# Kernel optimization log

Measured on AMD Instinct MI355X. Metric: run time of the kernel, lower is better.

## Reference

```python
import jax, jax.numpy as jnp
import numpy as np

BS, IN, H, G, E, A = 4096, 256, 256, 64, 256, 30
NW = IN * H  # hypernet-generated weight count per sample


def _ln(x, g, b, eps=1e-5):
    mu = jnp.mean(x, axis=-1, keepdims=True)
    var = jnp.mean(jnp.square(x - mu), axis=-1, keepdims=True)
    return (x - mu) * jax.lax.rsqrt(var + eps) * g + b


def setup_inputs() -> dict:
    key = jax.random.key(0)
    ks = jax.random.split(key, 24)
    sc = 0.02
    return {
        "inputs": jax.random.normal(ks[0], (BS, IN), jnp.float32),
        "hidden_state": jax.random.normal(ks[1], (BS, H), jnp.float32),
        "goal": jax.random.normal(ks[2], (BS, G), jnp.float32),
        "ln1_g": jnp.ones((IN,), jnp.float32),
        "ln1_b": jnp.zeros((IN,), jnp.float32),
        "hy_w1": jax.random.normal(ks[3], (E, G), jnp.float32) * sc,
        "hy_b1": jnp.zeros((E,), jnp.float32),
        "hy_w2": jax.random.normal(ks[4], (NW + H, E), jnp.float32) * sc,
        "hy_b2": jnp.zeros((NW + H,), jnp.float32),
        "ln2_g": jnp.ones((H,), jnp.float32),
        "ln2_b": jnp.zeros((H,), jnp.float32),
        "fe_w": jax.random.normal(ks[5], (H, H), jnp.float32) * sc,
        "fe_b": jnp.zeros((H,), jnp.float32),
        "w_ih": jax.random.normal(ks[6], (3 * H, H), jnp.float32) * sc,
        "w_hh": jax.random.normal(ks[7], (3 * H, H), jnp.float32) * sc,
        "b_ih": jnp.zeros((3 * H,), jnp.float32),
        "b_hh": jnp.zeros((3 * H,), jnp.float32),
        "val_w": jax.random.normal(ks[8], (1, H), jnp.float32) * sc,
        "val_b": jnp.zeros((1,), jnp.float32),
        "adv_w": jax.random.normal(ks[9], (A, H), jnp.float32) * sc,
        "adv_b": jnp.zeros((A,), jnp.float32),
    }


def reference(inputs, hidden_state, goal, ln1_g, ln1_b, hy_w1, hy_b1, hy_w2, hy_b2,
              ln2_g, ln2_b, fe_w, fe_b, w_ih, w_hh, b_ih, b_hh, val_w, val_b,
              adv_w, adv_b):
    x_in = _ln(inputs, ln1_g, ln1_b)  # [BS, IN]
    # hypernetwork: goal -> per-sample (weights, bias)
    h1 = jax.nn.relu(goal @ hy_w1.T + hy_b1)           # [BS, E]
    hyper = jnp.tanh(h1 @ hy_w2.T + hy_b2) * 3.0        # [BS, NW+H]
    weights = hyper[:, :NW].reshape(BS, IN, H)
    bias = hyper[:, NW:]                                 # [BS, H]
    x = jnp.einsum('bi,bih->bh', x_in, weights) + bias   # per-sample matmul
    x = _ln(x, ln2_g, ln2_b)
    x = jax.nn.relu(x) @ fe_w.T + fe_b                    # feat_extract_2
    # GRUCell
    h_in = hidden_state.reshape(-1, H)
    gi = x @ w_ih.T + b_ih
    gh = h_in @ w_hh.T + b_hh
    i_r, i_z, i_n = jnp.split(gi, 3, axis=1)
    h_r, h_z, h_n = jnp.split(gh, 3, axis=1)
    r = jax.nn.sigmoid(i_r + h_r)
    z = jax.nn.sigmoid(i_z + h_z)
    n = jnp.tanh(i_n + r * h_n)
    h = (1.0 - z) * n + z * h_in
    # dueling heads
    val = h @ val_w.T + val_b                             # [BS, 1]
    adv = h @ adv_w.T + adv_b                             # [BS, A]
    q = val + (adv - jnp.mean(adv, axis=1, keepdims=True))
    return q, h
```

## Files before the change

### kernel.cpp

```cpp
#include <hip/hip_runtime.h>
#include <hip/hip_bf16.h>

typedef unsigned short u16;
typedef __attribute__((ext_vector_type(4))) float f32x4;
typedef __attribute__((ext_vector_type(8))) short short8;
typedef __attribute__((ext_vector_type(8))) u16 u16x8;

__device__ __forceinline__ f32x4 fzero() { f32x4 z = {0.f, 0.f, 0.f, 0.f}; return z; }

__device__ __forceinline__ u16 f2b(float x) {
  unsigned u = __builtin_bit_cast(unsigned, x);
  unsigned r = (u + 0x7fffu + ((u >> 16) & 1u)) >> 16;
  return (u16)r;
}

#define BS 4096
#define H_ 256
#define A_ 30

#define OFF_W2B   0UL
#define OFF_HIDB  33685504UL
#define OFF_FWT   35782656UL
#define OFF_WIHB  35913728UL
#define OFF_WHHB  36306944UL
#define OFF_H1B   36700160UL
#define OFF_XIN   38797312UL
#define OFF_WCB   40894464UL
#define OFF_BCB   41287680UL
#define OFF_PART  42991616UL

#define NC_W2   2105344L
#define NC_HID  131072L
#define NC_FET  8192L
#define NC_WIH  24576L
#define NC_WHH  24576L
#define NB_CONV 8960
#define NB_PRE  (NB_CONV + 4096 + 4096)

__device__ __forceinline__ void blk_ln(float v, float* red, int t, float& mu, float& inv) {
  float s = v, sq = v * v;
  #pragma unroll
  for (int o = 32; o; o >>= 1) { s += __shfl_xor(s, o); sq += __shfl_xor(sq, o); }
  int w = t >> 6;
  if ((t & 63) == 0) { red[w] = s; red[4 + w] = sq; }
  __syncthreads();
  float S = red[0] + red[1] + red[2] + red[3];
  float Q = red[4] + red[5] + red[6] + red[7];
  mu = S * (1.f / 256.f);
  float var = Q * (1.f / 256.f) - mu * mu;
  inv = rsqrtf(var + 1e-5f);
  __syncthreads();
}

__global__ void k_pre(const float* __restrict__ hyw2, const float* __restrict__ hid,
                      const float* __restrict__ few,  const float* __restrict__ wih,
                      const float* __restrict__ whh,
                      const float* __restrict__ inp,  const float* __restrict__ ln1g,
                      const float* __restrict__ ln1b,
                      const float* __restrict__ goal, const float* __restrict__ hyw1,
                      const float* __restrict__ hyb1,
                      u16* __restrict__ w2b, u16* __restrict__ hidb, u16* __restrict__ fwbT,
                      u16* __restrict__ wihb, u16* __restrict__ whhb,
                      float* __restrict__ xin, u16* __restrict__ h1b) {
  const int bx = blockIdx.x, t = threadIdx.x;
  __shared__ float sm[64];

  if (bx < NB_CONV) {
    long c = (long)bx * 256 + t;
    if (c < NC_W2) {
      long d = c * 8;
      int kk0 = (int)((c & 3) * 8);
      int h   = (int)((c >> 2) & 255);
      long s  = c >> 10;
      int ks  = (int)(s & 7);
      long i  = s >> 3;
      const float* src = hyw2 + (i * 256 + h) * 256 + ks * 32 + kk0;
      f32x4 a = *(const f32x4*)src;
      f32x4 b = *(const f32x4*)(src + 4);
      u16x8 o;
      o[0]=f2b(a[0]); o[1]=f2b(a[1]); o[2]=f2b(a[2]); o[3]=f2b(a[3]);
      o[4]=f2b(b[0]); o[5]=f2b(b[1]); o[6]=f2b(b[2]); o[7]=f2b(b[3]);
      *(u16x8*)(w2b + d) = o;
      return;
    }
    c -= NC_W2;
    const float* src = nullptr; u16* dst = nullptr;
    if (c < NC_HID) { src = hid; dst = hidb; }
    else {
      c -= NC_HID;
      if (c < NC_FET) {
        long d = c * 8;
        int h = (int)(c >> 5), e0 = (int)((c & 31) * 8);
        u16x8 o;
        #pragma unroll
        for (int j = 0; j < 8; ++j) o[j] = f2b(few[(long)(e0 + j) * 256 + h]);
        *(u16x8*)(fwbT + d) = o;
        return;
      }
      c -= NC_FET;
      if (c < NC_WIH) { src = wih; dst = wihb; }
      else { c -= NC_WIH; src = whh; dst = whhb; }
    }
    long e = c * 8;
    f32x4 a = *(const f32x4*)(src + e);
    f32x4 b = *(const f32x4*)(src + e + 4);
    u16x8 o;
    o[0]=f2b(a[0]); o[1]=f2b(a[1]); o[2]=f2b(a[2]); o[3]=f2b(a[3]);
    o[4]=f2b(b[0]); o[5]=f2b(b[1]); o[6]=f2b(b[2]); o[7]=f2b(b[3]);
    *(u16x8*)(dst + e) = o;
    return;
  }

  if (bx < NB_CONV + 4096) {
    int bb = bx - NB_CONV;
    float v = inp[(long)bb * 256 + t];
    float mu, inv; blk_ln(v, sm, t, mu, inv);
    xin[(long)bb * 256 + t] = (v - mu) * inv * ln1g[t] + ln1b[t];
    return;
  }

  {
    int bb = bx - (NB_CONV + 4096);
    if (t < 64) sm[t] = goal[(long)bb * 64 + t];
    __syncthreads();
    const float* wr = hyw1 + (long)t * 64;
    float acc = hyb1[t];
    #pragma unroll
    for (int g4 = 0; g4 < 16; ++g4) {
      f32x4 w = *(const f32x4*)(wr + g4 * 4);
      acc = fmaf(sm[g4*4+0], w[0], acc);
      acc = fmaf(sm[g4*4+1], w[1], acc);
      acc = fmaf(sm[g4*4+2], w[2], acc);
      acc = fmaf(sm[g4*4+3], w[3], acc);
    }
    h1b[(long)bb * 256 + t] = f2b(fmaxf(acc, 0.f));
  }
}

__global__ __launch_bounds__(256, 2) void k_big(const u16* __restrict__ w2b,
                                                const u16* __restrict__ h1b,
                                                const float* __restrict__ xin,
                                                const float* __restrict__ b2,
                                                float* __restrict__ part) {
  const int bx = blockIdx.x;
  const int islice = bx & 7, btile = bx >> 3;
  const int b0 = btile * 64, i0 = islice * 32;
  const int ni = (islice == 7) ? 33 : 32;
  const int t = threadIdx.x, lane = t & 63, wid = t >> 6;
  const int la = lane & 15, lb = lane >> 4;
  const int c0 = wid * 64;

  __shared__ u16 As[64 * 264];
  __shared__ float xs[32][64];

  #pragma unroll
  for (int j = 0; j < 8; ++j) {
    int q = t + 256 * j;
    int row = q >> 5, cc = q & 31;
    *(u16x8*)&As[row * 264 + cc * 8] = *(const u16x8*)(h1b + (long)(b0 + row) * 256 + cc * 8);
  }
  {
    int row = t >> 2, part4 = t & 3;
    const float* src = xin + (long)(b0 + row) * 256 + i0 + part4 * 8;
    f32x4 v0 = *(const f32x4*)src;
    f32x4 v1 = *(const f32x4*)(src + 4);
    #pragma unroll
    for (int j = 0; j < 4; ++j) xs[part4 * 8 + j][row] = v0[j];
    #pragma unroll
    for (int j = 0; j < 4; ++j) xs[part4 * 8 + 4 + j][row] = v1[j];
  }
  __syncthreads();

  const u16* bptr = w2b + (long)i0 * 8 * 8192 + (c0 + la) * 32 + lb * 8;
  const int lds_a = la * 528 + lb * 16;

  f32x4 accT[4][4];
  #pragma unroll
  for (int m = 0; m < 4; ++m)
    #pragma unroll
    for (int n = 0; n < 4; ++n) accT[m][n] = fzero();

  short8 bf[4][4];
  #pragma unroll
  for (int s = 0; s < 4; ++s)
    #pragma unroll
    for (int n = 0; n < 4; ++n)
      bf[s][n] = *(const short8*)(bptr + (long)s * 8192 + n * 512);

  for (int ii = 0; ii < ni; ++ii) {
    f32x4 cf[4][4];
    #pragma unroll
    for (int ks = 0; ks < 8; ++ks) {
      const int s = ii * 8 + ks;
      __builtin_amdgcn_s_barrier();
      short8 af[4];
      #pragma unroll
      for (int m = 0; m < 4; ++m)
        af[m] = *(const short8*)((const char*)As + lds_a + m * 8448 + ks * 64);
      __builtin_amdgcn_s_setprio(1);
      if (ks == 0) {
        #pragma unroll
        for (int m = 0; m < 4; ++m)
          #pragma unroll
          for (int n = 0; n < 4; ++n)
            cf[m][n] = __builtin_amdgcn_mfma_f32_16x16x32_bf16(af[m], bf[ks & 3][n], fzero(), 0, 0, 0);
      } else {
        #pragma unroll
        for (int m = 0; m < 4; ++m)
          #pragma unroll
          for (int n = 0; n < 4; ++n)
            cf[m][n] = __builtin_amdgcn_mfma_f32_16x16x32_bf16(af[m], bf[ks & 3][n], cf[m][n], 0, 0, 0);
      }
      __builtin_amdgcn_s_setprio(0);
      #pragma unroll
      for (int n = 0; n < 4; ++n)
        bf[ks & 3][n] = *(const short8*)(bptr + (long)(s + 4) * 8192 + n * 512);
    }
    const int ig = i0 + ii;
    const bool isb = (ig == 256);
    f32x4 xv[4];
    if (isb) {
      #pragma unroll
      for (int m = 0; m < 4; ++m) { f32x4 o = {1.f,1.f,1.f,1.f}; xv[m] = o; }
    } else {
      #pragma unroll
      for (int m = 0; m < 4; ++m)
        xv[m] = *(const f32x4*)&xs[ii][m * 16 + lb * 4];
    }
    float b2v[4];
    #pragma unroll
    for (int n = 0; n < 4; ++n)
      b2v[n] = b2[(long)ig * 256 + c0 + n * 16 + la];
    #pragma unroll
    for (int m = 0; m < 4; ++m)
      #pragma unroll
      for (int n = 0; n < 4; ++n)
        #pragma unroll
        for (int r = 0; r < 4; ++r) {
          float pre = cf[m][n][r] + b2v[n];
          float t2 = pre * pre;
          float w = pre * fmaf(t2, fmaf(t2, fmaf(t2, -0.161905f, 0.4f), -1.0f), 3.0f);
          accT[m][n][r] = fmaf(xv[m][r], w, accT[m][n][r]);
        }
  }

  float* dst = part + (long)islice * (4096 * 256);
  #pragma unroll
  for (int m = 0; m < 4; ++m)
    #pragma unroll
    for (int n = 0; n < 4; ++n)
      #pragma unroll
      for (int r = 0; r < 4; ++r)
        __builtin_nontemporal_store(accT[m][n][r],
            &dst[(long)(b0 + m * 16 + lb * 4 + r) * 256 + (c0 + n * 16 + la)]);
}

__global__ void k_mid(const float* __restrict__ part, const float* __restrict__ g,
                      const float* __restrict__ b, u16* __restrict__ yb,
                      const float* __restrict__ wihf, const float* __restrict__ few,
                      u16* __restrict__ wcb,
                      const float* __restrict__ bih, const float* __restrict__ feb,
                      float* __restrict__ bcb) {
  const int bx = blockIdx.x, t = threadIdx.x;
  __shared__ float sm[256];
  if (bx < 4096) {
    float s = 0.f;
    #pragma unroll
    for (int sl = 0; sl < 8; ++sl) s += part[(long)sl * (4096 * 256) + (long)bx * 256 + t];
    float mu, inv; blk_ln(s, sm, t, mu, inv);
    float v = (s - mu) * inv * g[t] + b[t];
    yb[(long)bx * 256 + t] = f2b(fmaxf(v, 0.f));
    return;
  }
  if (bx < 4096 + 768) {
    int gg = bx - 4096;
    sm[t] = wihf[(long)gg * 256 + t];
    __syncthreads();
    float acc = 0.f;
    #pragma unroll 8
    for (int e = 0; e < 256; ++e) acc = fmaf(sm[e], few[(long)e * 256 + t], acc);
    wcb[(long)gg * 256 + t] = f2b(acc);
    return;
  }
  {
    int gg = (bx - 4864) * 256 + t;
    float acc = bih[gg];
    const float* wr = wihf + (long)gg * 256;
    #pragma unroll 8
    for (int e = 0; e < 256; ++e) acc = fmaf(wr[e], feb[e], acc);
    bcb[gg] = acc;
  }
}

__device__ __forceinline__ void gemm256(const u16* __restrict__ Ab, const u16* __restrict__ Bb,
                                        const float* __restrict__ bias, float* __restrict__ Cf,
                                        int N, int ntiles, int blk, u16* As, u16* Bs) {
  const int t = threadIdx.x;
  const int mt = blk / ntiles, nt = blk % ntiles;
  const int m0 = mt * 128, n0 = nt * 128;
  const int lane = t & 63, wid = t >> 6;
  const int la = lane & 15, lb = lane >> 4;
  const int r0 = (wid >> 1) * 64, c0 = (wid & 1) * 64;
  f32x4 acc[4][4];
  #pragma unroll
  for (int m = 0; m < 4; ++m)
    #pragma unroll
    for (int n = 0; n < 4; ++n) acc[m][n] = fzero();
  for (int kh = 0; kh < 2; ++kh) {
    #pragma unroll
    for (int j = 0; j < 8; ++j) {
      int q = t + 256 * j;
      int row = q >> 4, cc = q & 15;
      *(u16x8*)&As[row * 136 + cc * 8] = *(const u16x8*)(Ab + (long)(m0 + row) * 256 + kh * 128 + cc * 8);
      *(u16x8*)&Bs[row * 136 + cc * 8] = *(const u16x8*)(Bb + (long)(n0 + row) * 256 + kh * 128 + cc * 8);
    }
    __syncthreads();
    #pragma unroll
    for (int ks = 0; ks < 4; ++ks) {
      short8 af[4], bf[4];
      #pragma unroll
      for (int m = 0; m < 4; ++m) af[m] = *(const short8*)&As[(r0 + m * 16 + la) * 136 + ks * 32 + lb * 8];
      #pragma unroll
      for (int n = 0; n < 4; ++n) bf[n] = *(const short8*)&Bs[(c0 + n * 16 + la) * 136 + ks * 32 + lb * 8];
      #pragma unroll
      for (int m = 0; m < 4; ++m)
        #pragma unroll
        for (int n = 0; n < 4; ++n)
          acc[m][n] = __builtin_amdgcn_mfma_f32_16x16x32_bf16(af[m], bf[n], acc[m][n], 0, 0, 0);
    }
    __syncthreads();
  }
  #pragma unroll
  for (int n = 0; n < 4; ++n) {
    int gc = n0 + c0 + n * 16 + la;
    float bv = bias[gc];
    #pragma unroll
    for (int m = 0; m < 4; ++m) {
      int gr = m0 + r0 + m * 16 + lb * 4;
      #pragma unroll
      for (int r = 0; r < 4; ++r)
        Cf[(long)(gr + r) * N + gc] = acc[m][n][r] + bv;
    }
  }
}

__global__ __launch_bounds__(256) void k_gigh(const u16* __restrict__ yb, const u16* __restrict__ wcb,
                                              const float* __restrict__ bcb,
                                              const u16* __restrict__ hidb, const u16* __restrict__ whhb,
                                              const float* __restrict__ bhh,
                                              float* __restrict__ gim, float* __restrict__ ghm) {
  __shared__ u16 smem[2 * 128 * 136];
  const int bx = blockIdx.x;
  if (bx < 192) gemm256(yb,   wcb,  bcb, gim, 768, 6, bx,       smem, smem + 128 * 136);
  else          gemm256(hidb, whhb, bhh, ghm, 768, 6, bx - 192, smem, smem + 128 * 136);
}

__global__ void k_gru(const float* __restrict__ gi, const float* __restrict__ gh,
                      const float* __restrict__ hin,
                      const float* __restrict__ vw, const float* __restrict__ vb,
                      const float* __restrict__ aw, const float* __restrict__ ab,
                      float* __restrict__ qout, float* __restrict__ hout) {
  int bb = blockIdx.x, t = threadIdx.x;
  const float* gib = gi + (long)bb * 768;
  const float* ghb = gh + (long)bb * 768;
  float ir = gib[t], iz = gib[256 + t], inx = gib[512 + t];
  float hr = ghb[t], hz = ghb[256 + t], hn = ghb[512 + t];
  float hprev = hin[(long)bb * 256 + t];
  float r = 1.f / (1.f + expf(-(ir + hr)));
  float z = 1.f / (1.f + expf(-(iz + hz)));
  float n = tanhf(inx + r * hn);
  float h = (1.f - z) * n + z * hprev;
  hout[(long)bb * 256 + t] = h;
  __shared__ float hl[256];
  __shared__ float ov[32];
  __shared__ float mred;
  hl[t] = h;
  __syncthreads();
  int gidx = t >> 3, lg = t & 7;
  if (gidx < 31) {
    const float* wr = (gidx < 30) ? (aw + (long)gidx * 256) : vw;
    float p = 0.f;
    #pragma unroll 8
    for (int j = 0; j < 32; ++j) p += hl[lg + 8 * j] * wr[lg + 8 * j];
    p += __shfl_xor(p, 1); p += __shfl_xor(p, 2); p += __shfl_xor(p, 4);
    if (lg == 0) ov[gidx] = p + ((gidx < 30) ? ab[gidx] : vb[0]);
  }
  __syncthreads();
  if (t == 0) {
    float m = 0.f;
    #pragma unroll
    for (int a = 0; a < 30; ++a) m += ov[a];
    mred = m * (1.f / 30.f);
  }
  __syncthreads();
  if (t < 30) qout[(long)bb * 30 + t] = ov[30] + ov[t] - mred;
}

extern "C" void kernel_launch(void* const* d_in, const int* in_sizes, int n_in,
                              void* d_out, int out_size, void* d_ws, size_t ws_size,
                              hipStream_t stream) {
  const float* inputs = (const float*)d_in[0];
  const float* hidden = (const float*)d_in[1];
  const float* goal   = (const float*)d_in[2];
  const float* ln1g   = (const float*)d_in[3];
  const float* ln1b   = (const float*)d_in[4];
  const float* hyw1   = (const float*)d_in[5];
  const float* hyb1   = (const float*)d_in[6];
  const float* hyw2   = (const float*)d_in[7];
  const float* hyb2   = (const float*)d_in[8];
  const float* ln2g   = (const float*)d_in[9];
  const float* ln2b   = (const float*)d_in[10];
  const float* few    = (const float*)d_in[11];
  const float* feb    = (const float*)d_in[12];
  const float* wih    = (const float*)d_in[13];
  const float* whh    = (const float*)d_in[14];
  const float* bih    = (const float*)d_in[15];
  const float* bhh    = (const float*)d_in[16];
  const float* valw   = (const float*)d_in[17];
  const float* valb   = (const float*)d_in[18];
  const float* advw   = (const float*)d_in[19];
  const float* advb   = (const float*)d_in[20];

  char* ws = (char*)d_ws;
  u16* w2b   = (u16*)(ws + OFF_W2B);
  u16* hidb  = (u16*)(ws + OFF_HIDB);
  u16* fwbT  = (u16*)(ws + OFF_FWT);
  u16* wihb  = (u16*)(ws + OFF_WIHB);
  u16* whhb  = (u16*)(ws + OFF_WHHB);
  u16* h1b   = (u16*)(ws + OFF_H1B);
  float* xin = (float*)(ws + OFF_XIN);
  u16* yb    = (u16*)(ws + OFF_XIN);
  u16* wcb   = (u16*)(ws + OFF_WCB);
  float* bcb = (float*)(ws + OFF_BCB);
  float* prt = (float*)(ws + OFF_PART);
  float* gim = (float*)(ws + OFF_PART);
  float* ghm = (float*)(ws + OFF_PART + 12582912UL);
  float* qout = (float*)d_out;
  float* hout = qout + (long)BS * A_;

  k_pre<<<NB_PRE, 256, 0, stream>>>(hyw2, hidden, few, wih, whh,
                                    inputs, ln1g, ln1b, goal, hyw1, hyb1,
                                    w2b, hidb, fwbT, wihb, whhb, xin, h1b);
  k_big<<<512, 256, 0, stream>>>(w2b, h1b, xin, hyb2, prt);
  k_mid<<<4867, 256, 0, stream>>>(prt, ln2g, ln2b, yb, wih, few, wcb, bih, feb, bcb);
  k_gigh<<<384, 256, 0, stream>>>(yb, wcb, bcb, hidb, whhb, bhh, gim, ghm);
  k_gru<<<4096, 256, 0, stream>>>(gim, ghm, hidden, valw, valb, advw, advb, qout, hout);
}
```

Measured before the change: 376.1 us.

## Fuse LN2, GRU gate GEMMs, GRU cell and dueling heads into one kernel

Replaces the separate k_mid, k_gigh and k_gru kernels with a single k_post kernel. Each 16-row tile sums the partials, applies LN2+ReLU, runs both gate GEMMs with MFMA against pre-fragmented bf16 weights, applies the GRU cell and computes the dueling heads, so the gi/gh intermediates never go to global memory. The folded W_ih·fe_w weight and bias are now built inside k_pre, and the bf16 copy of the hidden state is made in shared memory instead. k_big also moves the x/bias loads and barrier to the top of each i-iteration. The risk is that k_post launches only 256 blocks, which may underuse the GPU, and its B-fragments are read directly from global memory.

```diff
diff --git a/kernel.cpp b/kernel.cpp
--- a/kernel.cpp
+++ b/kernel.cpp
@@ -15,27 +15,23 @@
 }
 
 #define BS 4096
-#define H_ 256
 #define A_ 30
 
 #define OFF_W2B   0UL
-#define OFF_HIDB  33685504UL
-#define OFF_FWT   35782656UL
-#define OFF_WIHB  35913728UL
-#define OFF_WHHB  36306944UL
-#define OFF_H1B   36700160UL
-#define OFF_XIN   38797312UL
-#define OFF_WCB   40894464UL
-#define OFF_BCB   41287680UL
-#define OFF_PART  42991616UL
+#define OFF_H1B   33685504UL
+#define OFF_XIN   35782656UL
+#define OFF_WCFR  39976960UL
+#define OFF_WHFR  40370176UL
+#define OFF_BC    40763392UL
+#define OFF_PART  40766464UL
 
 #define NC_W2   2105344L
-#define NC_HID  131072L
-#define NC_FET  8192L
-#define NC_WIH  24576L
-#define NC_WHH  24576L
-#define NB_CONV 8960
-#define NB_PRE  (NB_CONV + 4096 + 4096)
+#define NB_W2   8224
+#define NB_WHH  96
+#define NB_LN1  4096
+#define NB_H1   4096
+#define NB_WC   768
+#define NB_PRE  (NB_W2 + NB_WHH + NB_LN1 + NB_H1 + NB_WC)
 
 __device__ __forceinline__ void blk_ln(float v, float* red, int t, float& mu, float& inv) {
   float s = v, sq = v * v;
@@ -52,75 +48,59 @@
   __syncthreads();
 }
 
-__global__ void k_pre(const float* __restrict__ hyw2, const float* __restrict__ hid,
-                      const float* __restrict__ few,  const float* __restrict__ wih,
-                      const float* __restrict__ whh,
+__global__ void k_pre(const float* __restrict__ hyw2, const float* __restrict__ whh,
                       const float* __restrict__ inp,  const float* __restrict__ ln1g,
                       const float* __restrict__ ln1b,
                       const float* __restrict__ goal, const float* __restrict__ hyw1,
                       const float* __restrict__ hyb1,
-                      u16* __restrict__ w2b, u16* __restrict__ hidb, u16* __restrict__ fwbT,
-                      u16* __restrict__ wihb, u16* __restrict__ whhb,
-                      float* __restrict__ xin, u16* __restrict__ h1b) {
+                      const float* __restrict__ wih,  const float* __restrict__ few,
+                      const float* __restrict__ feb,  const float* __restrict__ bih,
+                      u16* __restrict__ w2b, u16* __restrict__ whfr,
+                      float* __restrict__ xin, u16* __restrict__ h1b,
+                      u16* __restrict__ wcfr, float* __restrict__ bcv) {
   const int bx = blockIdx.x, t = threadIdx.x;
-  __shared__ float sm[64];
-
-  if (bx < NB_CONV) {
+  __shared__ float sm[256];
+  __shared__ float red[8];
+
+  if (bx < NB_W2) {
     long c = (long)bx * 256 + t;
-    if (c < NC_W2) {
-      long d = c * 8;
-      int kk0 = (int)((c & 3) * 8);
-      int h   = (int)((c >> 2) & 255);
-      long s  = c >> 10;
-      int ks  = (int)(s & 7);
-      long i  = s >> 3;
-      const float* src = hyw2 + (i * 256 + h) * 256 + ks * 32 + kk0;
-      f32x4 a = *(const f32x4*)src;
-      f32x4 b = *(const f32x4*)(src + 4);
-      u16x8 o;
-      o[0]=f2b(a[0]); o[1]=f2b(a[1]); o[2]=f2b(a[2]); o[3]=f2b(a[3]);
-      o[4]=f2b(b[0]); o[5]=f2b(b[1]); o[6]=f2b(b[2]); o[7]=f2b(b[3]);
-      *(u16x8*)(w2b + d) = o;
-      return;
-    }
-    c -= NC_W2;
-    const float* src = nullptr; u16* dst = nullptr;
-    if (c < NC_HID) { src = hid; dst = hidb; }
-    else {
-      c -= NC_HID;
-      if (c < NC_FET) {
-        long d = c * 8;
-        int h = (int)(c >> 5), e0 = (int)((c & 31) * 8);
-        u16x8 o;
-        #pragma unroll
-        for (int j = 0; j < 8; ++j) o[j] = f2b(few[(long)(e0 + j) * 256 + h]);
-        *(u16x8*)(fwbT + d) = o;
-        return;
-      }
-      c -= NC_FET;
-      if (c < NC_WIH) { src = wih; dst = wihb; }
-      else { c -= NC_WIH; src = whh; dst = whhb; }
-    }
-    long e = c * 8;
-    f32x4 a = *(const f32x4*)(src + e);
-    f32x4 b = *(const f32x4*)(src + e + 4);
+    long d = c * 8;
+    int kk0 = (int)((c & 3) * 8);
+    int h   = (int)((c >> 2) & 255);
+    long s  = c >> 10;
+    int ks  = (int)(s & 7);
+    long i  = s >> 3;
+    const float* src = hyw2 + (i * 256 + h) * 256 + ks * 32 + kk0;
+    f32x4 a = *(const f32x4*)src;
+    f32x4 b = *(const f32x4*)(src + 4);
     u16x8 o;
     o[0]=f2b(a[0]); o[1]=f2b(a[1]); o[2]=f2b(a[2]); o[3]=f2b(a[3]);
     o[4]=f2b(b[0]); o[5]=f2b(b[1]); o[6]=f2b(b[2]); o[7]=f2b(b[3]);
-    *(u16x8*)(dst + e) = o;
+    *(u16x8*)(w2b + d) = o;
     return;
   }
-
-  if (bx < NB_CONV + 4096) {
-    int bb = bx - NB_CONV;
+  if (bx < NB_W2 + NB_WHH) {
+    int c = (bx - NB_W2) * 256 + t;
+    int ks = c / 3072, rem = c - ks * 3072;
+    int g = rem >> 2, kk0 = (rem & 3) * 8;
+    const float* src = whh + (long)g * 256 + ks * 32 + kk0;
+    f32x4 a = *(const f32x4*)src;
+    f32x4 b = *(const f32x4*)(src + 4);
+    u16x8 o;
+    o[0]=f2b(a[0]); o[1]=f2b(a[1]); o[2]=f2b(a[2]); o[3]=f2b(a[3]);
+    o[4]=f2b(b[0]); o[5]=f2b(b[1]); o[6]=f2b(b[2]); o[7]=f2b(b[3]);
+    *(u16x8*)(whfr + ((long)ks * 768 + g) * 32 + kk0) = o;
+    return;
+  }
+  if (bx < NB_W2 + NB_WHH + NB_LN1) {
+    int bb = bx - (NB_W2 + NB_WHH);
     float v = inp[(long)bb * 256 + t];
-    float mu, inv; blk_ln(v, sm, t, mu, inv);
+    float mu, inv; blk_ln(v, red, t, mu, inv);
     xin[(long)bb * 256 + t] = (v - mu) * inv * ln1g[t] + ln1b[t];
     return;
   }
-
-  {
-    int bb = bx - (NB_CONV + 4096);
+  if (bx < NB_W2 + NB_WHH + NB_LN1 + NB_H1) {
+    int bb = bx - (NB_W2 + NB_WHH + NB_LN1);
     if (t < 64) sm[t] = goal[(long)bb * 64 + t];
     __syncthreads();
     const float* wr = hyw1 + (long)t * 64;
@@ -134,6 +114,22 @@
       acc = fmaf(sm[g4*4+3], w[3], acc);
     }
     h1b[(long)bb * 256 + t] = f2b(fmaxf(acc, 0.f));
+    return;
+  }
+  {
+    int gg = bx - (NB_W2 + NB_WHH + NB_LN1 + NB_H1);
+    sm[t] = wih[(long)gg * 256 + t];
+    __syncthreads();
+    float acc = 0.f;
+    #pragma unroll 8
+    for (int e = 0; e < 256; ++e) acc = fmaf(sm[e], few[(long)e * 256 + t], acc);
+    wcfr[((long)(t >> 5) * 768 + gg) * 32 + (t & 31)] = f2b(acc);
+    float p = sm[t] * feb[t];
+    #pragma unroll
+    for (int o = 32; o; o >>= 1) p += __shfl_xor(p, o);
+    if ((t & 63) == 0) red[t >> 6] = p;
+    __syncthreads();
+    if (t == 0) bcv[gg] = bih[gg] + red[0] + red[1] + red[2] + red[3];
   }
 }
 
@@ -188,11 +184,27 @@
       bf[s][n] = *(const short8*)(bptr + (long)s * 8192 + n * 512);
 
   for (int ii = 0; ii < ni; ++ii) {
+    __builtin_amdgcn_s_barrier();
+    const int ig = i0 + ii;
+    const bool isb = (ig == 256);
+    f32x4 xv[4];
+    if (isb) {
+      #pragma unroll
+      for (int m = 0; m < 4; ++m) { f32x4 o = {1.f,1.f,1.f,1.f}; xv[m] = o; }
+    } else {
+      #pragma unroll
+      for (int m = 0; m < 4; ++m)
+        xv[m] = *(const f32x4*)&xs[ii][m * 16 + lb * 4];
+    }
+    float b2v[4];
+    #pragma unroll
+    for (int n = 0; n < 4; ++n)
+      b2v[n] = b2[(long)ig * 256 + c0 + n * 16 + la];
+
     f32x4 cf[4][4];
     #pragma unroll
     for (int ks = 0; ks < 8; ++ks) {
       const int s = ii * 8 + ks;
-      __builtin_amdgcn_s_barrier();
       short8 af[4];
       #pragma unroll
       for (int m = 0; m < 4; ++m)
@@ -216,21 +228,6 @@
       for (int n = 0; n < 4; ++n)
         bf[ks & 3][n] = *(const short8*)(bptr + (long)(s + 4) * 8192 + n * 512);
     }
-    const int ig = i0 + ii;
-    const bool isb = (ig == 256);
-    f32x4 xv[4];
-    if (isb) {
-      #pragma unroll
-      for (int m = 0; m < 4; ++m) { f32x4 o = {1.f,1.f,1.f,1.f}; xv[m] = o; }
-    } else {
-      #pragma unroll
-      for (int m = 0; m < 4; ++m)
-        xv[m] = *(const f32x4*)&xs[ii][m * 16 + lb * 4];
-    }
-    float b2v[4];
-    #pragma unroll
-    for (int n = 0; n < 4; ++n)
-      b2v[n] = b2[(long)ig * 256 + c0 + n * 16 + la];
     #pragma unroll
     for (int m = 0; m < 4; ++m)
       #pragma unroll
@@ -255,145 +252,160 @@
             &dst[(long)(b0 + m * 16 + lb * 4 + r) * 256 + (c0 + n * 16 + la)]);
 }
 
-__global__ void k_mid(const float* __restrict__ part, const float* __restrict__ g,
-                      const float* __restrict__ b, u16* __restrict__ yb,
-                      const float* __restrict__ wihf, const float* __restrict__ few,
-                      u16* __restrict__ wcb,
-                      const float* __restrict__ bih, const float* __restrict__ feb,
-                      float* __restrict__ bcb) {
+__global__ __launch_bounds__(256) void k_post(const float* __restrict__ part,
+                                              const float* __restrict__ ln2g,
+                                              const float* __restrict__ ln2b,
+                                              const u16* __restrict__ wcfr,
+                                              const u16* __restrict__ whfr,
+                                              const float* __restrict__ bcv,
+                                              const float* __restrict__ bhh,
+                                              const float* __restrict__ hidden,
+                                              const float* __restrict__ advw,
+                                              const float* __restrict__ advb,
+                                              const float* __restrict__ valw,
+                                              const float* __restrict__ valb,
+                                              float* __restrict__ qout,
+                                              float* __restrict__ hout) {
   const int bx = blockIdx.x, t = threadIdx.x;
-  __shared__ float sm[256];
-  if (bx < 4096) {
-    float s = 0.f;
-    #pragma unroll
-    for (int sl = 0; sl < 8; ++sl) s += part[(long)sl * (4096 * 256) + (long)bx * 256 + t];
-    float mu, inv; blk_ln(s, sm, t, mu, inv);
-    float v = (s - mu) * inv * g[t] + b[t];
-    yb[(long)bx * 256 + t] = f2b(fmaxf(v, 0.f));
-    return;
-  }
-  if (bx < 4096 + 768) {
-    int gg = bx - 4096;
-    sm[t] = wihf[(long)gg * 256 + t];
-    __syncthreads();
-    float acc = 0.f;
-    #pragma unroll 8
-    for (int e = 0; e < 256; ++e) acc = fmaf(sm[e], few[(long)e * 256 + t], acc);
-    wcb[(long)gg * 256 + t] = f2b(acc);
-    return;
-  }
-  {
-    int gg = (bx - 4864) * 256 + t;
-    float acc = bih[gg];
-    const float* wr = wihf + (long)gg * 256;
-    #pragma unroll 8
-    for (int e = 0; e < 256; ++e) acc = fmaf(wr[e], feb[e], acc);
-    bcb[gg] = acc;
-  }
-}
-
-__device__ __forceinline__ void gemm256(const u16* __restrict__ Ab, const u16* __restrict__ Bb,
-                                        const float* __restrict__ bias, float* __restrict__ Cf,
-                                        int N, int ntiles, int blk, u16* As, u16* Bs) {
-  const int t = threadIdx.x;
-  const int mt = blk / ntiles, nt = blk % ntiles;
-  const int m0 = mt * 128, n0 = nt * 128;
+  const int b0 = bx * 16;
+  __shared__ u16 ya[16 * 264];
+  __shared__ u16 ha[16 * 264];
+  __shared__ float hs[16 * 264];
+  __shared__ float ov[16][33];
+  __shared__ float ms[16];
+
+  {
+    const int r = t >> 4, ch = (t & 15) * 16;
+    const float* pb = part + (long)(b0 + r) * 256 + ch;
+    f32x4 s4[4];
+    #pragma unroll
+    for (int q = 0; q < 4; ++q) s4[q] = fzero();
+    #pragma unroll
+    for (int sl = 0; sl < 8; ++sl) {
+      const f32x4* ps = (const f32x4*)(pb + (long)sl * (4096 * 256));
+      #pragma unroll
+      for (int q = 0; q < 4; ++q) {
+        f32x4 v = __builtin_nontemporal_load(ps + q);
+        s4[q] += v;
+      }
+    }
+    float sv = 0.f, sq = 0.f;
+    #pragma unroll
+    for (int q = 0; q < 4; ++q)
+      #pragma unroll
+      for (int j = 0; j < 4; ++j) { float v = s4[q][j]; sv += v; sq += v * v; }
+    #pragma unroll
+    for (int o = 1; o < 16; o <<= 1) { sv += __shfl_xor(sv, o); sq += __shfl_xor(sq, o); }
+    float mu = sv * (1.f / 256.f);
+    float inv = rsqrtf(sq * (1.f / 256.f) - mu * mu + 1e-5f);
+    u16x8 o0, o1;
+    #pragma unroll
+    for (int q = 0; q < 4; ++q)
+      #pragma unroll
+      for (int j = 0; j < 4; ++j) {
+        int c = ch + q * 4 + j;
+        float v = (s4[q][j] - mu) * inv * ln2g[c] + ln2b[c];
+        v = fmaxf(v, 0.f);
+        if (q < 2) o0[q * 4 + j] = f2b(v); else o1[(q - 2) * 4 + j] = f2b(v);
+      }
+    *(u16x8*)&ya[r * 264 + ch] = o0;
+    *(u16x8*)&ya[r * 264 + ch + 8] = o1;
+  }
+  {
+    const int r = t >> 4, ch = (t & 15) * 16;
+    const float* hp = hidden + (long)(b0 + r) * 256 + ch;
+    u16x8 o0, o1;
+    #pragma unroll
+    for (int j = 0; j < 8; ++j) o0[j] = f2b(hp[j]);
+    #pragma unroll
+    for (int j = 0; j < 8; ++j) o1[j] = f2b(hp[8 + j]);
+    *(u16x8*)&ha[r * 264 + ch] = o0;
+    *(u16x8*)&ha[r * 264 + ch + 8] = o1;
+  }
+  __syncthreads();
+
   const int lane = t & 63, wid = t >> 6;
   const int la = lane & 15, lb = lane >> 4;
-  const int r0 = (wid >> 1) * 64, c0 = (wid & 1) * 64;
-  f32x4 acc[4][4];
-  #pragma unroll
-  for (int m = 0; m < 4; ++m)
-    #pragma unroll
-    for (int n = 0; n < 4; ++n) acc[m][n] = fzero();
-  for (int kh = 0; kh < 2; ++kh) {
-    #pragma unroll
-    for (int j = 0; j < 8; ++j) {
-      int q = t + 256 * j;
-      int row = q >> 4, cc = q & 15;
-      *(u16x8*)&As[row * 136 + cc * 8] = *(const u16x8*)(Ab + (long)(m0 + row) * 256 + kh * 128 + cc * 8);
-      *(u16x8*)&Bs[row * 136 + cc * 8] = *(const u16x8*)(Bb + (long)(n0 + row) * 256 + kh * 128 + cc * 8);
-    }
-    __syncthreads();
-    #pragma unroll
-    for (int ks = 0; ks < 4; ++ks) {
-      short8 af[4], bf[4];
-      #pragma unroll
-      for (int m = 0; m < 4; ++m) af[m] = *(const short8*)&As[(r0 + m * 16 + la) * 136 + ks * 32 + lb * 8];
-      #pragma unroll
-      for (int n = 0; n < 4; ++n) bf[n] = *(const short8*)&Bs[(c0 + n * 16 + la) * 136 + ks * 32 + lb * 8];
-      #pragma unroll
-      for (int m = 0; m < 4; ++m)
-        #pragma unroll
-        for (int n = 0; n < 4; ++n)
-          acc[m][n] = __builtin_amdgcn_mfma_f32_16x16x32_bf16(af[m], bf[n], acc[m][n], 0, 0, 0);
-    }
-    __syncthreads();
-  }
+  const int c0w = wid * 64;
+  f32x4 aR[4], aZ[4], aN[4], aH[4];
+  #pragma unroll
+  for (int n = 0; n < 4; ++n) { aR[n] = fzero(); aZ[n] = fzero(); aN[n] = fzero(); aH[n] = fzero(); }
+  #pragma unroll
+  for (int ks = 0; ks < 8; ++ks) {
+    short8 ay = *(const short8*)&ya[la * 264 + ks * 32 + lb * 8];
+    short8 ah = *(const short8*)&ha[la * 264 + ks * 32 + lb * 8];
+    #pragma unroll
+    for (int n = 0; n < 4; ++n) {
+      const int c = c0w + n * 16 + la;
+      const u16* wp = wcfr + ((long)ks * 768 + c) * 32 + lb * 8;
+      const u16* hp = whfr + ((long)ks * 768 + c) * 32 + lb * 8;
+      short8 bWr = *(const short8*)wp;
+      short8 bWz = *(const short8*)(wp + 256 * 32);
+      short8 bWn = *(const short8*)(wp + 512 * 32);
+      short8 bHr = *(const short8*)hp;
+      short8 bHz = *(const short8*)(hp + 256 * 32);
+      short8 bHn = *(const short8*)(hp + 512 * 32);
+      aR[n] = __builtin_amdgcn_mfma_f32_16x16x32_bf16(ay, bWr, aR[n], 0, 0, 0);
+      aR[n] = __builtin_amdgcn_mfma_f32_16x16x32_bf16(ah, bHr, aR[n], 0, 0, 0);
+      aZ[n] = __builtin_amdgcn_mfma_f32_16x16x32_bf16(ay, bWz, aZ[n], 0, 0, 0);
+      aZ[n] = __builtin_amdgcn_mfma_f32_16x16x32_bf16(ah, bHz, aZ[n], 0, 0, 0);
+      aN[n] = __builtin_amdgcn_mfma_f32_16x16x32_bf16(ay, bWn, aN[n], 0, 0, 0);
+      aH[n] = __builtin_amdgcn_mfma_f32_16x16x32_bf16(ah, bHn, aH[n], 0, 0, 0);
+    }
+  }
+
   #pragma unroll
   for (int n = 0; n < 4; ++n) {
-    int gc = n0 + c0 + n * 16 + la;
-    float bv = bias[gc];
-    #pragma unroll
-    for (int m = 0; m < 4; ++m) {
-      int gr = m0 + r0 + m * 16 + lb * 4;
-      #pragma unroll
-      for (int r = 0; r < 4; ++r)
-        Cf[(long)(gr + r) * N + gc] = acc[m][n][r] + bv;
-    }
-  }
-}
-
-__global__ __launch_bounds__(256) void k_gigh(const u16* __restrict__ yb, const u16* __restrict__ wcb,
-                                              const float* __restrict__ bcb,
-                                              const u16* __restrict__ hidb, const u16* __restrict__ whhb,
-                                              const float* __restrict__ bhh,
-                                              float* __restrict__ gim, float* __restrict__ ghm) {
-  __shared__ u16 smem[2 * 128 * 136];
-  const int bx = blockIdx.x;
-  if (bx < 192) gemm256(yb,   wcb,  bcb, gim, 768, 6, bx,       smem, smem + 128 * 136);
-  else          gemm256(hidb, whhb, bhh, ghm, 768, 6, bx - 192, smem, smem + 128 * 136);
-}
-
-__global__ void k_gru(const float* __restrict__ gi, const float* __restrict__ gh,
-                      const float* __restrict__ hin,
-                      const float* __restrict__ vw, const float* __restrict__ vb,
-                      const float* __restrict__ aw, const float* __restrict__ ab,
-                      float* __restrict__ qout, float* __restrict__ hout) {
-  int bb = blockIdx.x, t = threadIdx.x;
-  const float* gib = gi + (long)bb * 768;
-  const float* ghb = gh + (long)bb * 768;
-  float ir = gib[t], iz = gib[256 + t], inx = gib[512 + t];
-  float hr = ghb[t], hz = ghb[256 + t], hn = ghb[512 + t];
-  float hprev = hin[(long)bb * 256 + t];
-  float r = 1.f / (1.f + expf(-(ir + hr)));
-  float z = 1.f / (1.f + expf(-(iz + hz)));
-  float n = tanhf(inx + r * hn);
-  float h = (1.f - z) * n + z * hprev;
-  hout[(long)bb * 256 + t] = h;
-  __shared__ float hl[256];
-  __shared__ float ov[32];
-  __shared__ float mred;
-  hl[t] = h;
-  __syncthreads();
-  int gidx = t >> 3, lg = t & 7;
-  if (gidx < 31) {
-    const float* wr = (gidx < 30) ? (aw + (long)gidx * 256) : vw;
-    float p = 0.f;
-    #pragma unroll 8
-    for (int j = 0; j < 32; ++j) p += hl[lg + 8 * j] * wr[lg + 8 * j];
-    p += __shfl_xor(p, 1); p += __shfl_xor(p, 2); p += __shfl_xor(p, 4);
-    if (lg == 0) ov[gidx] = p + ((gidx < 30) ? ab[gidx] : vb[0]);
-  }
-  __syncthreads();
-  if (t == 0) {
-    float m = 0.f;
-    #pragma unroll
-    for (int a = 0; a < 30; ++a) m += ov[a];
-    mred = m * (1.f / 30.f);
-  }
-  __syncthreads();
-  if (t < 30) qout[(long)bb * 30 + t] = ov[30] + ov[t] - mred;
+    const int c = c0w + n * 16 + la;
+    float bcr = bcv[c], bcz = bcv[c + 256], bcn = bcv[c + 512];
+    float bhr = bhh[c], bhz = bhh[c + 256], bhn = bhh[c + 512];
+    #pragma unroll
+    for (int jr = 0; jr < 4; ++jr) {
+      const int row = lb * 4 + jr;
+      const long gb = (long)(b0 + row) * 256 + c;
+      float rr = 1.f / (1.f + expf(-(aR[n][jr] + bcr + bhr)));
+      float zz = 1.f / (1.f + expf(-(aZ[n][jr] + bcz + bhz)));
+      float nn = tanhf(aN[n][jr] + bcn + rr * (aH[n][jr] + bhn));
+      float hp = hidden[gb];
+      float h = (1.f - zz) * nn + zz * hp;
+      hout[gb] = h;
+      hs[row * 264 + c] = h;
+    }
+  }
+  __syncthreads();
+
+  {
+    const int out = t >> 3, lg = t & 7;
+    if (out < 31) {
+      const float* wr = (out < 30) ? (advw + (long)out * 256) : valw;
+      for (int r = 0; r < 16; ++r) {
+        float p = 0.f;
+        #pragma unroll 8
+        for (int j = 0; j < 32; ++j) p += hs[r * 264 + lg + 8 * j] * wr[lg + 8 * j];
+        p += __shfl_xor(p, 1); p += __shfl_xor(p, 2); p += __shfl_xor(p, 4);
+        if (lg == 0) ov[r][out] = p + ((out < 30) ? advb[out] : valb[0]);
+      }
+    }
+  }
+  __syncthreads();
+  {
+    const int r = t >> 4, o = t & 15;
+    if (o == 0) {
+      float m = 0.f;
+      #pragma unroll
+      for (int a = 0; a < 30; ++a) m += ov[r][a];
+      ms[r] = m * (1.f / 30.f);
+    }
+  }
+  __syncthreads();
+  {
+    const int r = t >> 4, o = t & 15;
+    if (o < 15) {
+      float vv = ov[r][30], mm = ms[r];
+      qout[(long)(b0 + r) * 30 + o]      = vv + ov[r][o]      - mm;
+      qout[(long)(b0 + r) * 30 + o + 15] = vv + ov[r][o + 15] - mm;
+    }
+  }
 }
 
 extern "C" void kernel_launch(void* const* d_in, const int* in_sizes, int n_in,
@@ -422,27 +434,20 @@
   const float* advb   = (const float*)d_in[20];
 
   char* ws = (char*)d_ws;
-  u16* w2b   = (u16*)(ws + OFF_W2B);
-  u16* hidb  = (u16*)(ws + OFF_HIDB);
-  u16* fwbT  = (u16*)(ws + OFF_FWT);
-  u16* wihb  = (u16*)(ws + OFF_WIHB);
-  u16* whhb  = (u16*)(ws + OFF_WHHB);
-  u16* h1b   = (u16*)(ws + OFF_H1B);
-  float* xin = (float*)(ws + OFF_XIN);
-  u16* yb    = (u16*)(ws + OFF_XIN);
-  u16* wcb   = (u16*)(ws + OFF_WCB);
-  float* bcb = (float*)(ws + OFF_BCB);
-  float* prt = (float*)(ws + OFF_PART);
-  float* gim = (float*)(ws + OFF_PART);
-  float* ghm = (float*)(ws + OFF_PART + 12582912UL);
+  u16* w2b    = (u16*)(ws + OFF_W2B);
+  u16* h1b    = (u16*)(ws + OFF_H1B);
+  float* xin  = (float*)(ws + OFF_XIN);
+  u16* wcfr   = (u16*)(ws + OFF_WCFR);
+  u16* whfr   = (u16*)(ws + OFF_WHFR);
+  float* bcv  = (float*)(ws + OFF_BC);
+  float* prt  = (float*)(ws + OFF_PART);
   float* qout = (float*)d_out;
   float* hout = qout + (long)BS * A_;
 
-  k_pre<<<NB_PRE, 256, 0, stream>>>(hyw2, hidden, few, wih, whh,
-                                    inputs, ln1g, ln1b, goal, hyw1, hyb1,
-                                    w2b, hidb, fwbT, wihb, whhb, xin, h1b);
+  k_pre<<<NB_PRE, 256, 0, stream>>>(hyw2, whh, inputs, ln1g, ln1b, goal, hyw1, hyb1,
+                                    wih, few, feb, bih,
+                                    w2b, whfr, xin, h1b, wcfr, bcv);
   k_big<<<512, 256, 0, stream>>>(w2b, h1b, xin, hyb2, prt);
-  k_mid<<<4867, 256, 0, stream>>>(prt, ln2g, ln2b, yb, wih, few, wcb, bih, feb, bcb);
-  k_gigh<<<384, 256, 0, stream>>>(yb, wcb, bcb, hidb, whhb, bhh, gim, ghm);
-  k_gru<<<4096, 256, 0, stream>>>(gim, ghm, hidden, valw, valb, advw, advb, qout, hout);
-}
+  k_post<<<256, 256, 0, stream>>>(prt, ln2g, ln2b, wcfr, whfr, bcv, bhh, hidden,
+                                  advw, advb, valw, valb, qout, hout);
+}
```

Result: faster. 367.6 us (-2.3%).
